# Optimization experiments

Hardware: AMD Instinct MI355X
Metric: run time of the kernel (lower is better)

## Reference

```python
import jax, jax.numpy as jnp
import numpy as np

ROPE_BASE = 10000.0


def rotate_half(x):
    # interleaved rotate: (x0,x1,x2,x3,...) -> (-x1,x0,-x3,x2,...)
    x1 = x[..., ::2]
    x2 = x[..., 1::2]
    return jnp.stack((-x2, x1), axis=-1).reshape(x.shape)


def rope_cos_sin(seq_len, dim, dtype):
    inv_freq = 1.0 / (ROPE_BASE ** (jnp.arange(0, dim, 2, dtype=jnp.float32) / dim))
    pos = jnp.arange(seq_len, dtype=jnp.float32)
    freqs = jnp.outer(pos, inv_freq)              # [S, dim/2]
    emb = jnp.concatenate([freqs, freqs], axis=-1)  # [S, dim]
    return jnp.cos(emb).astype(dtype), jnp.sin(emb).astype(dtype)


def setup_inputs() -> dict:
    key = jax.random.key(0)
    k1, k2, k3, k4 = jax.random.split(key, 4)
    B, S, D = 4, 4096, 256
    scale = 1.0 / np.sqrt(D)
    x = jax.random.normal(k1, (B, S, D), dtype=jnp.float32)
    wq = jax.random.normal(k2, (D, D), dtype=jnp.float32) * scale
    wk = jax.random.normal(k3, (D, D), dtype=jnp.float32) * scale
    wv = jax.random.normal(k4, (D, D), dtype=jnp.float32) * scale
    return {"x": x, "wq": wq, "wk": wk, "wv": wv}


def reference(x, wq, wk, wv):
    D = x.shape[-1]
    S = x.shape[-2]
    # torch Linear: y = x @ W^T
    q = jnp.einsum('bsd,ed->bse', x, wq)
    k = jnp.einsum('bsd,ed->bse', x, wk)
    v = jnp.einsum('bsd,ed->bse', x, wv)
    cos, sin = rope_cos_sin(S, D, x.dtype)  # [S, D]
    q = q * cos + rotate_half(q) * sin
    k = k * cos + rotate_half(k) * sin
    scores = jnp.einsum('bqd,bkd->bqk', q, k) / jnp.sqrt(jnp.asarray(D, x.dtype))
    weights = jax.nn.softmax(scores, axis=-1)
    output = jnp.einsum('bqk,bkd->bqd', weights, v)
    return output, weights
```

## Files before the change

kernel.cpp:

```cpp
#include <hip/hip_runtime.h>
#include <hip/hip_bf16.h>
#include <stdint.h>


#define B_ 4
#define S_ 4096
#define D_ 256
#define NQ 4194304
#define NW 65536
#define NTAB 524288

typedef __attribute__((ext_vector_type(4))) float f32x4;
typedef __attribute__((ext_vector_type(8))) short short8;
typedef __attribute__((ext_vector_type(4))) short short4v;
typedef __attribute__((ext_vector_type(4))) unsigned uint32x4;

__device__ __forceinline__ short f2bf(float f) {
  unsigned u = __builtin_bit_cast(unsigned, f);
  u += 0x7fffu + ((u >> 16) & 1u);
  return (short)(u >> 16);
}
__device__ __forceinline__ float bf2f(short h) {
  unsigned u = ((unsigned)(unsigned short)h) << 16;
  return __builtin_bit_cast(float, u);
}

__device__ __forceinline__ void gload16(const void* g, void* l) {
  __builtin_amdgcn_global_load_lds(
      (const __attribute__((address_space(1))) unsigned*)g,
      (__attribute__((address_space(3))) unsigned*)l, 16, 0, 0);
}

__global__ __launch_bounds__(256) void k0_split(
    const float* __restrict__ x, const float* __restrict__ wq,
    const float* __restrict__ wk, const float* __restrict__ wv,
    short* __restrict__ xh, short* __restrict__ xl,
    short* __restrict__ wh, short* __restrict__ wl,
    float* __restrict__ ctab) {
  int idx = blockIdx.x * 256 + threadIdx.x;
  if (idx < NQ) {
    float v = x[idx];
    short hi = f2bf(v);
    xh[idx] = hi;
    xl[idx] = f2bf(v - bf2f(hi));
  } else if (idx < NQ + 3 * NW) {
    int r = idx - NQ;
    int m = r >> 16;
    int e = r & (NW - 1);
    const float* w = (m == 0) ? wq : (m == 1) ? wk : wv;
    float v = w[e];
    short hi = f2bf(v);
    wh[r] = hi;
    wl[r] = f2bf(v - bf2f(hi));
  } else {
    int t = idx - NQ - 3 * NW;
    int s = t >> 7, j = t & 127;
    float invf = __expf(-0.07195578415606394f * (float)j);
    float sn, cs;
    sincosf((float)s * invf, &sn, &cs);
    ctab[2 * t] = cs;
    ctab[2 * t + 1] = sn;
  }
}

__global__ __launch_bounds__(256) void k1_proj(
    const short* __restrict__ xh, const short* __restrict__ xl,
    const short* __restrict__ wh, const short* __restrict__ wl,
    const float* __restrict__ ctab,
    short* __restrict__ qh, short* __restrict__ ql,
    short* __restrict__ kh, short* __restrict__ kl,
    short* __restrict__ vt) {
  const int m = blockIdx.y;
  const int b = blockIdx.x >> 6;
  const int sbase = (blockIdx.x & 63) << 6;
  const int tid = threadIdx.x;
  const int w = tid >> 6;
  const int lane = tid & 63;
  const int lr = lane & 15;
  const int g = lane >> 4;

  const int srow = sbase + w * 16 + lr;
  const short* xhp = xh + ((size_t)(b * S_ + srow)) * D_;
  const short* xlp = xl + ((size_t)(b * S_ + srow)) * D_;
  const short* whm = wh + m * NW;
  const short* wlm = wl + m * NW;

  f32x4 acc[16];
#pragma unroll
  for (int i = 0; i < 16; ++i) acc[i] = (f32x4)0.f;

#pragma unroll
  for (int dc = 0; dc < 8; ++dc) {
    const int d = dc * 32 + g * 8;
    short8 ah = *(const short8*)(xhp + d);
    short8 al = *(const short8*)(xlp + d);
#pragma unroll
    for (int ct = 0; ct < 16; ++ct) {
      const int e = ct * 16 + lr;
      short8 bh = *(const short8*)(whm + e * D_ + d);
      short8 bl = *(const short8*)(wlm + e * D_ + d);
      acc[ct] = __builtin_amdgcn_mfma_f32_16x16x32_bf16(ah, bh, acc[ct], 0, 0, 0);
      acc[ct] = __builtin_amdgcn_mfma_f32_16x16x32_bf16(ah, bl, acc[ct], 0, 0, 0);
      acc[ct] = __builtin_amdgcn_mfma_f32_16x16x32_bf16(al, bh, acc[ct], 0, 0, 0);
    }
  }

  const int s0 = sbase + w * 16 + g * 4;
  if (m == 2) {
#pragma unroll
    for (int ct = 0; ct < 16; ++ct) {
      const int e = ct * 16 + lr;
      short4v pk;
#pragma unroll
      for (int r = 0; r < 4; ++r) pk[r] = f2bf(acc[ct][r]);
      *(short4v*)(vt + ((size_t)(b * D_ + e)) * S_ + s0) = pk;
    }
  } else {
    short* oh = (m == 0) ? qh : kh;
    short* ol = (m == 0) ? ql : kl;
#pragma unroll
    for (int ct = 0; ct < 16; ++ct) {
      const int e = ct * 16 + lr;
      const float sgn = (e & 1) ? 1.0f : -1.0f;
#pragma unroll
      for (int r = 0; r < 4; ++r) {
        float v = acc[ct][r];
        float p = __shfl_xor(v, 1, 64);
        const float2 cs2 = *(const float2*)(ctab + ((size_t)((s0 + r) << 7) + (e & 127)) * 2);
        float q2 = v * cs2.x + sgn * p * cs2.y;
        short hi = f2bf(q2);
        size_t off = ((size_t)(b * S_ + s0 + r)) * D_ + e;
        oh[off] = hi;
        ol[off] = f2bf(q2 - bf2f(hi));
      }
    }
  }
}

__global__ __launch_bounds__(256, 2) void k2_fused(
    const short* __restrict__ qh, const short* __restrict__ ql,
    const short* __restrict__ kh, const short* __restrict__ kl,
    const short* __restrict__ vt,
    float* __restrict__ wts, float* __restrict__ out) {
  __shared__ __align__(16) char kbuf[65536];
  __shared__ __align__(16) char etile[2][2048];
  float* partA = (float*)(kbuf + 49152);
  float* lsumA = (float*)(kbuf + 50176);

  const int bid = blockIdx.x;
  const int swz = (bid & 7) * 64 + ((bid >> 3) & 31) * 2 + (bid >> 8);
  const int b = swz >> 7;
  const int qbase = (swz & 127) << 5;
  const int tid = threadIdx.x;
  const int w = tid >> 6;
  const int lane = tid & 63;
  const int lr = lane & 15;
  const int g = lane >> 4;
  const int qg = w & 1;
  const int kg = w >> 1;

  short8 qfh[8], qfl[8];
  {
    const int qrow = qbase + qg * 16 + lr;
    const short* ph = qh + ((size_t)(b * S_ + qrow)) * D_;
    const short* pl = ql + ((size_t)(b * S_ + qrow)) * D_;
#pragma unroll
    for (int dc = 0; dc < 8; ++dc) {
      qfh[dc] = *(const short8*)(ph + dc * 32 + g * 8);
      qfl[dc] = *(const short8*)(pl + dc * 32 + g * 8);
    }
  }

  f32x4 acc = (f32x4)0.f;
  f32x4 accv[2][4];
#pragma unroll
  for (int qs = 0; qs < 2; ++qs)
#pragma unroll
    for (int dt = 0; dt < 4; ++dt) accv[qs][dt] = (f32x4)0.f;
  float rs = 0.f;

  const char* khb = (const char*)(kh + (size_t)b * S_ * D_);
  const char* klb = (const char*)(kl + (size_t)b * S_ * D_);
  const short* vtb = vt + (size_t)b * D_ * S_;
  const int swx = (lane & 7) << 4;

  char* WB = (char*)(wts + ((size_t)(b * S_ + qbase)) * S_);
  char* EB = WB + 262144;

  auto STAGE = [&](int kt, char* dst) {
#pragma unroll
    for (int i = 0; i < 4; ++i) {
      const int p = i * 4096 + tid * 16;
      const int xo = p ^ (((p >> 9) & 7) << 4);
      gload16(khb + (size_t)kt * 16384 + xo, dst + p);
      gload16(klb + (size_t)kt * 16384 + xo, dst + 16384 + p);
    }
  };

  STAGE(0, kbuf);
  __syncthreads();

  for (int kt = 0; kt < 128; ++kt) {
    const int cur = kt & 1;
    const char* kb = kbuf + cur * 32768;

    if (kt < 127) STAGE(kt + 1, kbuf + (cur ^ 1) * 32768);

    if (kt > 0) {
      const char* et = etile[cur ^ 1];
      {
        const int p = tid * 8;
        const int row = p >> 6, cb = p & 63;
        uint2 v = *(const uint2*)(et + (p ^ ((row & 3) << 4)));
        *(uint2*)(EB + (size_t)row * 8192 + (kt - 1) * 64 + cb) = v;
      }
      __builtin_amdgcn_s_setprio(1);
      short8 ea0 = *(const short8*)(et + ((lr * 64 + g * 16) ^ ((lr & 3) << 4)));
      short8 ea1 = *(const short8*)(et + (((16 + lr) * 64 + g * 16) ^ ((lr & 3) << 4)));
#pragma unroll
      for (int dt = 0; dt < 4; ++dt) {
        const int d = w * 64 + dt * 16 + lr;
        short8 vb = *(const short8*)(vtb + (size_t)d * S_ + (kt - 1) * 32 + g * 8);
        accv[0][dt] = __builtin_amdgcn_mfma_f32_16x16x32_bf16(ea0, vb, accv[0][dt], 0, 0, 0);
        accv[1][dt] = __builtin_amdgcn_mfma_f32_16x16x32_bf16(ea1, vb, accv[1][dt], 0, 0, 0);
      }
      __builtin_amdgcn_s_setprio(0);
    }

    __builtin_amdgcn_s_setprio(1);
#pragma unroll
    for (int dc = 0; dc < 8; ++dc) {
      const int row = kg * 16 + lr;
      const int x = (row * 512 + dc * 64 + g * 16) ^ swx;
      short8 afh = *(const short8*)(kb + x);
      short8 afl = *(const short8*)(kb + 16384 + x);
      acc = __builtin_amdgcn_mfma_f32_16x16x32_bf16(afh, qfh[dc], acc, 0, 0, 0);
      acc = __builtin_amdgcn_mfma_f32_16x16x32_bf16(afh, qfl[dc], acc, 0, 0, 0);
      acc = __builtin_amdgcn_mfma_f32_16x16x32_bf16(afl, qfh[dc], acc, 0, 0, 0);
    }
    __builtin_amdgcn_s_setprio(0);

    {
      f32x4 e;
#pragma unroll
      for (int r = 0; r < 4; ++r) e[r] = __expf(acc[r] * 0.0625f);
      rs += e[0] + e[1] + e[2] + e[3];
      unsigned lo = (unsigned)(unsigned short)f2bf(e[0]) |
                    ((unsigned)(unsigned short)f2bf(e[1]) << 16);
      unsigned hi2 = (unsigned)(unsigned short)f2bf(e[2]) |
                     ((unsigned)(unsigned short)f2bf(e[3]) << 16);
      const int row = qg * 16 + lr;
      const int colb = (kg * 16 + g * 4) * 2;
      const int ad = (row * 64 + colb) ^ ((row & 3) << 4);
      *(uint2*)(etile[cur] + ad) = make_uint2(lo, hi2);
      acc = (f32x4)0.f;
    }
    __syncthreads();
  }

  {
    const char* et = etile[1];
    {
      const int p = tid * 8;
      const int row = p >> 6, cb = p & 63;
      uint2 v = *(const uint2*)(et + (p ^ ((row & 3) << 4)));
      *(uint2*)(EB + (size_t)row * 8192 + 127 * 64 + cb) = v;
    }
    short8 ea0 = *(const short8*)(et + ((lr * 64 + g * 16) ^ ((lr & 3) << 4)));
    short8 ea1 = *(const short8*)(et + (((16 + lr) * 64 + g * 16) ^ ((lr & 3) << 4)));
#pragma unroll
    for (int dt = 0; dt < 4; ++dt) {
      const int d = w * 64 + dt * 16 + lr;
      short8 vb = *(const short8*)(vtb + (size_t)d * S_ + 127 * 32 + g * 8);
      accv[0][dt] = __builtin_amdgcn_mfma_f32_16x16x32_bf16(ea0, vb, accv[0][dt], 0, 0, 0);
      accv[1][dt] = __builtin_amdgcn_mfma_f32_16x16x32_bf16(ea1, vb, accv[1][dt], 0, 0, 0);
    }
  }

  rs += __shfl_xor(rs, 16, 64);
  rs += __shfl_xor(rs, 32, 64);
  if (lane < 16) partA[kg * 32 + qg * 16 + lane] = rs;
  __syncthreads();
  if (tid < 32) lsumA[tid] = partA[tid] + partA[32 + tid];
  __syncthreads();

#pragma unroll
  for (int i = 0; i < 4; ++i) {
    const int p = i * 4096 + tid * 16;
    *(uint32x4*)(kbuf + p) = *(const uint32x4*)(EB + (size_t)30 * 8192 + p);
  }

  {
    float* ob = out + (size_t)b * S_ * D_;
    float rv[2][4];
#pragma unroll
    for (int qs = 0; qs < 2; ++qs)
#pragma unroll
      for (int r = 0; r < 4; ++r)
        rv[qs][r] = 1.0f / lsumA[qs * 16 + g * 4 + r];
#pragma unroll
    for (int qs = 0; qs < 2; ++qs)
#pragma unroll
      for (int dt = 0; dt < 4; ++dt)
#pragma unroll
        for (int r = 0; r < 4; ++r) {
          const int q = qbase + qs * 16 + g * 4 + r;
          ob[(size_t)q * D_ + w * 64 + dt * 16 + lr] = accv[qs][dt][r] * rv[qs][r];
        }
  }
  __syncthreads();

  const int pr0[5] = {0, 16, 24, 28, 30};
  const int pr1[5] = {16, 24, 28, 30, 32};
  float* WBf = (float*)WB;
#pragma unroll 1
  for (int ph = 0; ph < 5; ++ph) {
    for (int r = pr0[ph] + w; r < pr1[ph]; r += 4) {
      const float rinv = 1.0f / lsumA[r];
      const short* erow = (r >= 30) ? (const short*)(kbuf + (size_t)(r - 30) * 8192)
                                    : (const short*)(EB + (size_t)r * 8192);
      float* wrow = WBf + (size_t)r * 4096;
      for (int c = lane * 8; c < 4096; c += 512) {
        short8 ev = *(const short8*)(erow + c);
        f32x4 o0, o1;
#pragma unroll
        for (int j = 0; j < 4; ++j) o0[j] = bf2f(ev[j]) * rinv;
#pragma unroll
        for (int j = 0; j < 4; ++j) o1[j] = bf2f(ev[4 + j]) * rinv;
        *(f32x4*)(wrow + c) = o0;
        *(f32x4*)(wrow + c + 4) = o1;
      }
    }
    __syncthreads();
  }
}

extern "C" void kernel_launch(void* const* d_in, const int* in_sizes, int n_in,
                              void* d_out, int out_size, void* d_ws, size_t ws_size,
                              hipStream_t stream) {
  const float* x  = (const float*)d_in[0];
  const float* wq = (const float*)d_in[1];
  const float* wk = (const float*)d_in[2];
  const float* wv = (const float*)d_in[3];

  float* out = (float*)d_out;
  float* wts = out + (size_t)B_ * S_ * D_;

  short* xh = (short*)d_ws;
  short* xl = xh + NQ;
  short* qh = xl + NQ;
  short* ql = qh + NQ;
  short* kh = ql + NQ;
  short* kl = kh + NQ;
  short* vt = kl + NQ;
  short* wh = vt + NQ;
  short* wl = wh + 3 * NW;
  float* ctab = (float*)(wl + 3 * NW);

  k0_split<<<dim3((NQ + 3 * NW + NTAB) / 256), 256, 0, stream>>>(
      x, wq, wk, wv, xh, xl, wh, wl, ctab);
  k1_proj<<<dim3(B_ * S_ / 64, 3), 256, 0, stream>>>(
      xh, xl, wh, wl, ctab, qh, ql, kh, kl, vt);
  k2_fused<<<dim3(512), 256, 0, stream>>>(
      qh, ql, kh, kl, vt, wts, out);
}
```

Measured before the change: 446.4 us.

## Recompute attention weights in second pass instead of staging bf16 exps through output

Keys are stored as a single bf16 part (the low-order K correction is dropped), so the QK^T product now uses two MFMAs per chunk instead of three and K staging halves its shared-memory footprint. The old approach wrote bf16 exp tiles into a scratch area of the weights output and then reread and rescaled them. That is replaced by a second pass over K that recomputes the scores and writes normalized fp32 weights directly once the row sums are known. This removes the scratch round trip and the extra K low-part traffic, but doubles the QK^T compute and lowers score precision on the K side.

```diff
diff --git a/kernel.cpp b/kernel.cpp
--- a/kernel.cpp
+++ b/kernel.cpp
@@ -68,8 +68,7 @@
     const short* __restrict__ wh, const short* __restrict__ wl,
     const float* __restrict__ ctab,
     short* __restrict__ qh, short* __restrict__ ql,
-    short* __restrict__ kh, short* __restrict__ kl,
-    short* __restrict__ vt) {
+    short* __restrict__ kh, short* __restrict__ vt) {
   const int m = blockIdx.y;
   const int b = blockIdx.x >> 6;
   const int sbase = (blockIdx.x & 63) << 6;
@@ -117,7 +116,6 @@
     }
   } else {
     short* oh = (m == 0) ? qh : kh;
-    short* ol = (m == 0) ? ql : kl;
 #pragma unroll
     for (int ct = 0; ct < 16; ++ct) {
       const int e = ct * 16 + lr;
@@ -131,7 +129,7 @@
         short hi = f2bf(q2);
         size_t off = ((size_t)(b * S_ + s0 + r)) * D_ + e;
         oh[off] = hi;
-        ol[off] = f2bf(q2 - bf2f(hi));
+        if (m == 0) ql[off] = f2bf(q2 - bf2f(hi));
       }
     }
   }
@@ -139,13 +137,12 @@
 
 __global__ __launch_bounds__(256, 2) void k2_fused(
     const short* __restrict__ qh, const short* __restrict__ ql,
-    const short* __restrict__ kh, const short* __restrict__ kl,
-    const short* __restrict__ vt,
+    const short* __restrict__ kh, const short* __restrict__ vt,
     float* __restrict__ wts, float* __restrict__ out) {
-  __shared__ __align__(16) char kbuf[65536];
+  __shared__ __align__(16) char kbuf[32768];
   __shared__ __align__(16) char etile[2][2048];
-  float* partA = (float*)(kbuf + 49152);
-  float* lsumA = (float*)(kbuf + 50176);
+  __shared__ float part[2][32];
+  __shared__ float lsum_l[32];
 
   const int bid = blockIdx.x;
   const int swz = (bid & 7) * 64 + ((bid >> 3) & 31) * 2 + (bid >> 8);
@@ -180,12 +177,10 @@
   float rs = 0.f;
 
   const char* khb = (const char*)(kh + (size_t)b * S_ * D_);
-  const char* klb = (const char*)(kl + (size_t)b * S_ * D_);
   const short* vtb = vt + (size_t)b * D_ * S_;
   const int swx = (lane & 7) << 4;
 
-  char* WB = (char*)(wts + ((size_t)(b * S_ + qbase)) * S_);
-  char* EB = WB + 262144;
+  float* WBf = wts + ((size_t)(b * S_ + qbase)) * S_;
 
   auto STAGE = [&](int kt, char* dst) {
 #pragma unroll
@@ -193,7 +188,6 @@
       const int p = i * 4096 + tid * 16;
       const int xo = p ^ (((p >> 9) & 7) << 4);
       gload16(khb + (size_t)kt * 16384 + xo, dst + p);
-      gload16(klb + (size_t)kt * 16384 + xo, dst + 16384 + p);
     }
   };
 
@@ -202,18 +196,12 @@
 
   for (int kt = 0; kt < 128; ++kt) {
     const int cur = kt & 1;
-    const char* kb = kbuf + cur * 32768;
-
-    if (kt < 127) STAGE(kt + 1, kbuf + (cur ^ 1) * 32768);
+    const char* kb = kbuf + cur * 16384;
+
+    if (kt < 127) STAGE(kt + 1, kbuf + (cur ^ 1) * 16384);
 
     if (kt > 0) {
       const char* et = etile[cur ^ 1];
-      {
-        const int p = tid * 8;
-        const int row = p >> 6, cb = p & 63;
-        uint2 v = *(const uint2*)(et + (p ^ ((row & 3) << 4)));
-        *(uint2*)(EB + (size_t)row * 8192 + (kt - 1) * 64 + cb) = v;
-      }
       __builtin_amdgcn_s_setprio(1);
       short8 ea0 = *(const short8*)(et + ((lr * 64 + g * 16) ^ ((lr & 3) << 4)));
       short8 ea1 = *(const short8*)(et + (((16 + lr) * 64 + g * 16) ^ ((lr & 3) << 4)));
@@ -233,10 +221,8 @@
       const int row = kg * 16 + lr;
       const int x = (row * 512 + dc * 64 + g * 16) ^ swx;
       short8 afh = *(const short8*)(kb + x);
-      short8 afl = *(const short8*)(kb + 16384 + x);
       acc = __builtin_amdgcn_mfma_f32_16x16x32_bf16(afh, qfh[dc], acc, 0, 0, 0);
       acc = __builtin_amdgcn_mfma_f32_16x16x32_bf16(afh, qfl[dc], acc, 0, 0, 0);
-      acc = __builtin_amdgcn_mfma_f32_16x16x32_bf16(afl, qfh[dc], acc, 0, 0, 0);
     }
     __builtin_amdgcn_s_setprio(0);
 
@@ -260,12 +246,6 @@
 
   {
     const char* et = etile[1];
-    {
-      const int p = tid * 8;
-      const int row = p >> 6, cb = p & 63;
-      uint2 v = *(const uint2*)(et + (p ^ ((row & 3) << 4)));
-      *(uint2*)(EB + (size_t)row * 8192 + 127 * 64 + cb) = v;
-    }
     short8 ea0 = *(const short8*)(et + ((lr * 64 + g * 16) ^ ((lr & 3) << 4)));
     short8 ea1 = *(const short8*)(et + (((16 + lr) * 64 + g * 16) ^ ((lr & 3) << 4)));
 #pragma unroll
@@ -279,16 +259,10 @@
 
   rs += __shfl_xor(rs, 16, 64);
   rs += __shfl_xor(rs, 32, 64);
-  if (lane < 16) partA[kg * 32 + qg * 16 + lane] = rs;
+  if (lane < 16) part[kg][qg * 16 + lane] = rs;
   __syncthreads();
-  if (tid < 32) lsumA[tid] = partA[tid] + partA[32 + tid];
+  if (tid < 32) lsum_l[tid] = part[0][tid] + part[1][tid];
   __syncthreads();
-
-#pragma unroll
-  for (int i = 0; i < 4; ++i) {
-    const int p = i * 4096 + tid * 16;
-    *(uint32x4*)(kbuf + p) = *(const uint32x4*)(EB + (size_t)30 * 8192 + p);
-  }
 
   {
     float* ob = out + (size_t)b * S_ * D_;
@@ -297,7 +271,7 @@
     for (int qs = 0; qs < 2; ++qs)
 #pragma unroll
       for (int r = 0; r < 4; ++r)
-        rv[qs][r] = 1.0f / lsumA[qs * 16 + g * 4 + r];
+        rv[qs][r] = 1.0f / lsum_l[qs * 16 + g * 4 + r];
 #pragma unroll
     for (int qs = 0; qs < 2; ++qs)
 #pragma unroll
@@ -308,29 +282,36 @@
           ob[(size_t)q * D_ + w * 64 + dt * 16 + lr] = accv[qs][dt][r] * rv[qs][r];
         }
   }
+
+  const float rinvw = 1.0f / lsum_l[qg * 16 + lr];
+  float* wrow = WBf + (size_t)(qg * 16 + lr) * S_ + kg * 16 + g * 4;
+
+  STAGE(0, kbuf);
   __syncthreads();
 
-  const int pr0[5] = {0, 16, 24, 28, 30};
-  const int pr1[5] = {16, 24, 28, 30, 32};
-  float* WBf = (float*)WB;
-#pragma unroll 1
-  for (int ph = 0; ph < 5; ++ph) {
-    for (int r = pr0[ph] + w; r < pr1[ph]; r += 4) {
-      const float rinv = 1.0f / lsumA[r];
-      const short* erow = (r >= 30) ? (const short*)(kbuf + (size_t)(r - 30) * 8192)
-                                    : (const short*)(EB + (size_t)r * 8192);
-      float* wrow = WBf + (size_t)r * 4096;
-      for (int c = lane * 8; c < 4096; c += 512) {
-        short8 ev = *(const short8*)(erow + c);
-        f32x4 o0, o1;
-#pragma unroll
-        for (int j = 0; j < 4; ++j) o0[j] = bf2f(ev[j]) * rinv;
-#pragma unroll
-        for (int j = 0; j < 4; ++j) o1[j] = bf2f(ev[4 + j]) * rinv;
-        *(f32x4*)(wrow + c) = o0;
-        *(f32x4*)(wrow + c + 4) = o1;
-      }
-    }
+  for (int kt = 0; kt < 128; ++kt) {
+    const int cur = kt & 1;
+    const char* kb = kbuf + cur * 16384;
+
+    if (kt < 127) STAGE(kt + 1, kbuf + (cur ^ 1) * 16384);
+
+    f32x4 a2 = (f32x4)0.f;
+    __builtin_amdgcn_s_setprio(1);
+#pragma unroll
+    for (int dc = 0; dc < 8; ++dc) {
+      const int row = kg * 16 + lr;
+      const int x = (row * 512 + dc * 64 + g * 16) ^ swx;
+      short8 afh = *(const short8*)(kb + x);
+      a2 = __builtin_amdgcn_mfma_f32_16x16x32_bf16(afh, qfh[dc], a2, 0, 0, 0);
+      a2 = __builtin_amdgcn_mfma_f32_16x16x32_bf16(afh, qfl[dc], a2, 0, 0, 0);
+    }
+    __builtin_amdgcn_s_setprio(0);
+
+    f32x4 wv;
+#pragma unroll
+    for (int r = 0; r < 4; ++r) wv[r] = __expf(a2[r] * 0.0625f) * rinvw;
+    *(f32x4*)(wrow + kt * 32) = wv;
+
     __syncthreads();
   }
 }
@@ -351,8 +332,7 @@
   short* qh = xl + NQ;
   short* ql = qh + NQ;
   short* kh = ql + NQ;
-  short* kl = kh + NQ;
-  short* vt = kl + NQ;
+  short* vt = kh + NQ;
   short* wh = vt + NQ;
   short* wl = wh + 3 * NW;
   float* ctab = (float*)(wl + 3 * NW);
@@ -360,7 +340,7 @@
   k0_split<<<dim3((NQ + 3 * NW + NTAB) / 256), 256, 0, stream>>>(
       x, wq, wk, wv, xh, xl, wh, wl, ctab);
   k1_proj<<<dim3(B_ * S_ / 64, 3), 256, 0, stream>>>(
-      xh, xl, wh, wl, ctab, qh, ql, kh, kl, vt);
+      xh, xl, wh, wl, ctab, qh, ql, kh, vt);
   k2_fused<<<dim3(512), 256, 0, stream>>>(
-      qh, ql, kh, kl, vt, wts, out);
-}
+      qh, ql, kh, vt, wts, out);
+}
```

After: 473.0 us. 6.0% more time.
